# Optimization experiments

Hardware: AMD Instinct MI355X
Metric: run time of the kernel (lower is better)

## Reference

```python
import jax, jax.numpy as jnp
import numpy as np

VOCAB = 1024
EMBED_DIM = 64
COMMIT_COST = 0.25


def setup_inputs() -> dict:
    key = jax.random.key(0)
    k1, k2 = jax.random.split(key)
    z_e = jax.random.normal(k1, (64, 64, 32, 32), dtype=jnp.float32)
    # nn.Embedding init: uniform(-1/vocab, 1/vocab)
    embedding = jax.random.uniform(
        k2, (VOCAB, EMBED_DIM), dtype=jnp.float32,
        minval=-1.0 / VOCAB, maxval=1.0 / VOCAB)
    return {"z_e": z_e, "embedding": embedding}


def reference(z_e, embedding):
    b, d, h, w = z_e.shape
    # [B,D,H,W] -> [N,D]
    flat_z = jnp.transpose(z_e, (0, 2, 3, 1)).reshape(-1, d)
    # squared L2 distances to each code: [N, V]
    distances = (
        jnp.sum(flat_z * flat_z, axis=1, keepdims=True)
        + jnp.sum(embedding * embedding, axis=1)
        - 2.0 * flat_z @ embedding.T
    )
    flat_indices = jnp.argmin(distances, axis=1)
    indices = flat_indices.reshape(b, h, w)
    # gather codes and restore [B,D,H,W]
    z_q = embedding[flat_indices].reshape(b, h, w, d)
    z_q = jnp.transpose(z_q, (0, 3, 1, 2))
    quantization_loss = jnp.mean((z_q - jax.lax.stop_gradient(z_e)) ** 2)
    commitment_loss = jnp.mean((z_e - jax.lax.stop_gradient(z_q)) ** 2) * COMMIT_COST
    z_q_st = z_e + jax.lax.stop_gradient(z_q - z_e)
    # perplexity over codebook usage
    counts = jnp.zeros((VOCAB,), dtype=jnp.float32).at[flat_indices].add(1.0)
    avg_probs = counts / flat_indices.shape[0]
    perplexity = jnp.exp(-jnp.sum(avg_probs * jnp.log(avg_probs + 1e-10)))
    return (z_q_st, indices, quantization_loss, commitment_loss, perplexity)
```

## Files before the change

### kernel.cpp

```cpp
#include <hip/hip_runtime.h>
#include <math.h>

#define VOCAB 1024
#define ED 64
#define NROWS 65536
#define NELEM 4194304
#define MARGIN 2.0e-4f
#define CAPF 8192

typedef __attribute__((ext_vector_type(8))) short short8;
typedef __attribute__((ext_vector_type(4))) float f32x4;

__device__ __forceinline__ unsigned f2bf(float f) {
    unsigned u = __float_as_uint(f);
    u += 0x7fff + ((u >> 16) & 1);
    return u >> 16;
}

__device__ __forceinline__ unsigned long long packkey(float d, int c) {
    unsigned f = __float_as_uint(d);
    unsigned sd = (f & 0x80000000u) ? ~f : (f | 0x80000000u);
    return ((unsigned long long)sd << 32) | (unsigned)c;
}


__global__ void vq_prep(const float* __restrict__ emb, float* __restrict__ e2f,
                        uint4* __restrict__ FB, unsigned* __restrict__ zw1,
                        unsigned* __restrict__ zw2) {
    const int tid = blockIdx.x * 256 + threadIdx.x;
    for (int i = tid; i < 1028; i += 2048) zw1[i] = 0u;
    for (int i = tid; i < 2560; i += 2048) zw2[i] = 0u;

    if (tid < VOCAB) {
        const float4* src = (const float4*)(emb + tid * ED);
        double s = 0.0;
        #pragma unroll
        for (int g = 0; g < 16; ++g) {
            float4 f = src[g];
            s = fma((double)f.x, (double)f.x, s);
            s = fma((double)f.y, (double)f.y, s);
            s = fma((double)f.z, (double)f.z, s);
            s = fma((double)f.w, (double)f.w, s);
        }
        e2f[tid] = (float)s;
    }
    #pragma unroll
    for (int e = 0; e < 4; ++e) {
        const int i = e * 2048 + tid;
        const int n = i & 15, q = (i >> 4) & 3, kh = (i >> 6) & 1, T = i >> 7;
        const int code = T * 16 + n;
        const int k0 = kh * 32 + q * 8;
        const float4* sp = (const float4*)(emb + code * 64 + k0);
        float4 f0 = sp[0], f1 = sp[1];
        uint4 pk;
        pk.x = f2bf(f0.x) | (f2bf(f0.y) << 16);
        pk.y = f2bf(f0.z) | (f2bf(f0.w) << 16);
        pk.z = f2bf(f1.x) | (f2bf(f1.y) << 16);
        pk.w = f2bf(f1.z) | (f2bf(f1.w) << 16);
        FB[i] = pk;
    }
}

__global__ __launch_bounds__(256, 2)
void vq_filter(const float* __restrict__ z, const float* __restrict__ emb,
               const float* __restrict__ e2f, const uint4* __restrict__ FB,
               float* __restrict__ out, double* __restrict__ lossp,
               unsigned* __restrict__ hist, unsigned* __restrict__ nflag,
               unsigned* __restrict__ rowlist) {
    __shared__ uint4 Bs4[4096];
    __shared__ float e2s[1024];
    __shared__ float rowb1[128], rowb2[128];
    __shared__ int   rowi1[128], rowfl[128];
    __shared__ double wls[4];

    const int t = threadIdx.x;
    const int w = t >> 6, lane = t & 63;
    const int q = lane >> 4, n_lo = lane & 15;
    const int bk = blockIdx.x;
    const int n0 = bk * 128;
    const int b  = n0 >> 10;
    const int sb = n0 & 1023;

    #pragma unroll
    for (int i = 0; i < 4; ++i) e2s[i * 256 + t] = e2f[i * 256 + t];

    short8 af[2][2];
    #pragma unroll
    for (int rt = 0; rt < 2; ++rt) {
        const int s = sb + w * 32 + rt * 16 + n_lo;
        const float* zp = z + (size_t)b * 65536 + s;
        #pragma unroll
        for (int kh = 0; kh < 2; ++kh) {
            short8 fr;
            #pragma unroll
            for (int j = 0; j < 8; ++j) {
                int d = kh * 32 + q * 8 + j;
                fr[j] = (short)f2bf(-2.0f * zp[d * 1024]);
            }
            af[rt][kh] = fr;
        }
    }

    float b1[8], b2[8]; int i1[8];
    #pragma unroll
    for (int sl = 0; sl < 8; ++sl) { b1[sl] = 3.4e38f; b2[sl] = 3.4e38f; i1[sl] = 0; }

    const short8* FBs = (const short8*)Bs4;
    for (int h = 0; h < 2; ++h) {
        __syncthreads();
        {
            const uint4* src = FB + h * 4096;
            #pragma unroll
            for (int i = 0; i < 16; ++i) Bs4[i * 256 + t] = src[i * 256 + t];
        }
        __syncthreads();
        #pragma unroll 2
        for (int tt = 0; tt < 32; ++tt) {
            const int T = h * 32 + tt;
            short8 bf0 = FBs[tt * 128 + lane];
            short8 bf1 = FBs[tt * 128 + 64 + lane];
            const int cb = T * 16 + n_lo;
            const float e2 = e2s[cb];
            #pragma unroll
            for (int rt = 0; rt < 2; ++rt) {
                f32x4 a; a[0] = e2; a[1] = e2; a[2] = e2; a[3] = e2;
                a = __builtin_amdgcn_mfma_f32_16x16x32_bf16(af[rt][0], bf0, a, 0, 0, 0);
                a = __builtin_amdgcn_mfma_f32_16x16x32_bf16(af[rt][1], bf1, a, 0, 0, 0);
                #pragma unroll
                for (int reg = 0; reg < 4; ++reg) {
                    const int sl = rt * 4 + reg;
                    float s0 = a[reg];
                    b2[sl] = __builtin_amdgcn_fmed3f(s0, b1[sl], b2[sl]);
                    bool lt = s0 < b1[sl];
                    i1[sl] = lt ? cb : i1[sl];
                    b1[sl] = lt ? s0 : b1[sl];
                }
            }
        }
    }

    #pragma unroll
    for (int m = 1; m < 16; m <<= 1) {
        #pragma unroll
        for (int sl = 0; sl < 8; ++sl) {
            float ob1 = __shfl_xor(b1[sl], m, 64);
            int   oi1 = __shfl_xor(i1[sl], m, 64);
            float ob2 = __shfl_xor(b2[sl], m, 64);
            float lose = fmaxf(b1[sl], ob1);
            b2[sl] = fminf(fminf(b2[sl], ob2), lose);
            bool take = (ob1 < b1[sl]) || (ob1 == b1[sl] && oi1 < i1[sl]);
            b1[sl] = take ? ob1 : b1[sl];
            i1[sl] = take ? oi1 : i1[sl];
        }
    }
    if (n_lo == 0) {
        #pragma unroll
        for (int rt = 0; rt < 2; ++rt) {
            #pragma unroll
            for (int reg = 0; reg < 4; ++reg) {
                int row = w * 32 + rt * 16 + q * 4 + reg;
                int sl = rt * 4 + reg;
                rowb1[row] = b1[sl];
                rowb2[row] = b2[sl];
                rowi1[row] = i1[sl];
            }
        }
    }
    __syncthreads();

    if (t < 128) {
        const int nrow = n0 + t;
        const int code = rowi1[t];
        const bool want = rowb2[t] < rowb1[t] + MARGIN;
        unsigned long long mask = __ballot(want);
        const int cnt = __popcll(mask);
        unsigned base = 0;
        if (lane == 0 && cnt > 0) base = atomicAdd(nflag, (unsigned)cnt);
        base = (unsigned)__shfl((int)base, 0, 64);
        int f = 0;
        if (want) {
            const int rank = __popcll(mask & ((1ULL << lane) - 1ULL));
            const unsigned slot = base + (unsigned)rank;
            if (slot < CAPF) { rowlist[slot] = (unsigned)nrow; f = 1; }
        }
        rowfl[t] = f;
        out[NELEM + nrow] = (float)code;
        if (!f) atomicAdd(&hist[code], 1u);
    }
    __syncthreads();

    {
        const int r = t & 127, tg = t >> 7;
        const int code2 = rowi1[r];
        const bool fl2 = rowfl[r] != 0;
        const int scol = sb + r;
        double lsum = 0.0;
        #pragma unroll
        for (int i = 0; i < 8; ++i) {
            const int d4 = tg * 8 + i;
            float4 e4 = *(const float4*)(emb + code2 * 64 + d4 * 4);
            float es[4] = {e4.x, e4.y, e4.z, e4.w};
            #pragma unroll
            for (int j = 0; j < 4; ++j) {
                int d = d4 * 4 + j;
                size_t off = (size_t)b * 65536 + (size_t)d * 1024 + scol;
                float zv = z[off];
                out[off] = zv + (es[j] - zv);
                double df = (double)es[j] - (double)zv;
                lsum = fma(df, df, lsum);
            }
        }
        if (fl2) lsum = 0.0;
        #pragma unroll
        for (int off = 32; off > 0; off >>= 1)
            lsum += __shfl_down(lsum, off, 64);
        if (lane == 0) wls[w] = lsum;
    }
    __syncthreads();
    if (t == 0) lossp[bk] = wls[0] + wls[1] + wls[2] + wls[3];
}

#define EDOT(i) { \
    const f32x4 a4 = *(const f32x4*)(za + (i) * 4); \
    const f32x4 b4 = *(const f32x4*)(zb + (i) * 4); \
    ma = fmaf(a4[0], e##i[0], ma); ma = fmaf(a4[1], e##i[1], ma); \
    ma = fmaf(a4[2], e##i[2], ma); ma = fmaf(a4[3], e##i[3], ma); \
    mb = fmaf(b4[0], e##i[0], mb); mb = fmaf(b4[1], e##i[1], mb); \
    mb = fmaf(b4[2], e##i[2], mb); mb = fmaf(b4[3], e##i[3], mb); }

__global__ __launch_bounds__(512, 1)
void vq_rescue(const float* __restrict__ z, const float* __restrict__ emb,
               const float* __restrict__ e2f, float* __restrict__ out,
               double* __restrict__ lossp2, unsigned* __restrict__ hist,
               const unsigned* __restrict__ nflag,
               const unsigned* __restrict__ rowlist) {
    __shared__ float zs[32 * 64];
    __shared__ float zns[32];
    __shared__ unsigned long long wkey[16][32];
    __shared__ int rbi[32];
    __shared__ double lred[8];

    const int t = threadIdx.x, w = t >> 6, lane = t & 63;
    const int g = blockIdx.x;
    unsigned nfr = *nflag;
    const int nf = (int)(nfr < CAPF ? nfr : CAPF);
    if (g * 32 >= nf) return;
    const int nloc = (nf - g * 32 < 32) ? (nf - g * 32) : 32;

    {
        const int r = t >> 4, k0 = (t & 15) * 4;
        if (r < nloc) {
            const int row = (int)rowlist[g * 32 + r];
            const int bb = row >> 10, s = row & 1023;
            const float* zp = z + (size_t)bb * 65536 + s;
            #pragma unroll
            for (int k = 0; k < 4; ++k)
                zs[r * 64 + k0 + k] = zp[(size_t)(k0 + k) * 1024];
        }
    }
    __syncthreads();

    if (t < nloc) {
        double a = 0.0;
        for (int k = 0; k < 64; ++k) {
            double v = (double)zs[t * 64 + k];
            a = fma(v, v, a);
        }
        zns[t] = (float)a;
    }
    __syncthreads();

    for (int pass = 0; pass < 2; ++pass) {
        const int c = pass * 512 + w * 64 + lane;
        const f32x4* ep = (const f32x4*)(emb + (size_t)c * 64);
        f32x4 e0 = ep[0],  e1 = ep[1],  e2 = ep[2],  e3 = ep[3];
        f32x4 e4 = ep[4],  e5 = ep[5],  e6 = ep[6],  e7 = ep[7];
        f32x4 e8 = ep[8],  e9 = ep[9],  e10 = ep[10], e11 = ep[11];
        f32x4 e12 = ep[12], e13 = ep[13], e14 = ep[14], e15 = ep[15];
        const float e2c = e2f[c];

        for (int r0 = 0; r0 < nloc; r0 += 2) {
            const bool two = (r0 + 1 < nloc);
            const float* za = zs + r0 * 64;
            const float* zb = zs + (two ? r0 + 1 : r0) * 64;
            float ma = 0.f, mb = 0.f;
            EDOT(0)  EDOT(1)  EDOT(2)  EDOT(3)
            EDOT(4)  EDOT(5)  EDOT(6)  EDOT(7)
            EDOT(8)  EDOT(9)  EDOT(10) EDOT(11)
            EDOT(12) EDOT(13) EDOT(14) EDOT(15)

            const float da = (zns[r0] + e2c) - 2.0f * ma;
            unsigned long long ka = packkey(da, c);
            #pragma unroll
            for (int mo = 32; mo > 0; mo >>= 1) {
                unsigned long long o = __shfl_xor(ka, mo, 64);
                if (o < ka) ka = o;
            }
            unsigned long long kb2 = 0;
            if (two) {
                const float db = (zns[r0 + 1] + e2c) - 2.0f * mb;
                kb2 = packkey(db, c);
                #pragma unroll
                for (int mo = 32; mo > 0; mo >>= 1) {
                    unsigned long long o = __shfl_xor(kb2, mo, 64);
                    if (o < kb2) kb2 = o;
                }
            }
            if (lane == 0) {
                wkey[pass * 8 + w][r0] = ka;
                if (two) wkey[pass * 8 + w][r0 + 1] = kb2;
            }
        }
    }
    __syncthreads();

    if (t < nloc) {
        unsigned long long k0 = wkey[0][t];
        #pragma unroll
        for (int i = 1; i < 16; ++i) {
            unsigned long long ki = wkey[i][t];
            if (ki < k0) k0 = ki;
        }
        const int code = (int)(unsigned)(k0 & 0xffffffffu);
        rbi[t] = code;
        const int row = (int)rowlist[g * 32 + t];
        out[NELEM + row] = (float)code;
        atomicAdd(&hist[code], 1u);
    }
    __syncthreads();

    double lsum = 0.0;
    if (t < 256) {
        const int r = t >> 3, d0 = (t & 7) * 8;
        if (r < nloc) {
            const int row = (int)rowlist[g * 32 + r];
            const int bb = row >> 10, s = row & 1023;
            const int code = rbi[r];
            float4 ea = *(const float4*)(emb + code * 64 + d0);
            float4 eb = *(const float4*)(emb + code * 64 + d0 + 4);
            float es[8] = {ea.x, ea.y, ea.z, ea.w, eb.x, eb.y, eb.z, eb.w};
            #pragma unroll
            for (int j = 0; j < 8; ++j) {
                const int d = d0 + j;
                const size_t off = (size_t)bb * 65536 + (size_t)d * 1024 + s;
                const float zv = zs[r * 64 + d];
                out[off] = zv + (es[j] - zv);
                double df = (double)es[j] - (double)zv;
                lsum = fma(df, df, lsum);
            }
        }
    }
    #pragma unroll
    for (int o = 32; o > 0; o >>= 1) lsum += __shfl_down(lsum, o, 64);
    if (lane == 0) lred[w] = lsum;
    __syncthreads();
    if (t == 0) {
        double s = 0.0;
        #pragma unroll
        for (int i = 0; i < 8; ++i) s += lred[i];
        lossp2[g] = s;
    }
}

__global__ void vq_finalize_kernel(const unsigned* __restrict__ hist,
                                   const double* __restrict__ lossp,
                                   const double* __restrict__ lossp2,
                                   float* __restrict__ out) {
    __shared__ double red[256], red2[256];
    int t = threadIdx.x;
    double ssum = 0.0, lsum = 0.0;
    for (int i = t; i < VOCAB; i += 256) {
        double p = (double)hist[i] / (double)NROWS;
        ssum += p * log(p + 1e-10);
    }
    for (int i = t; i < 1024; i += 256) lsum += lossp[i];
    lsum += lossp2[t];
    red[t] = ssum; red2[t] = lsum;
    __syncthreads();
    for (int off = 128; off > 0; off >>= 1) {
        if (t < off) { red[t] += red[t + off]; red2[t] += red2[t + off]; }
        __syncthreads();
    }
    if (t == 0) {
        double qv = red2[0] / (double)NELEM;
        out[NELEM + NROWS + 0] = (float)qv;
        out[NELEM + NROWS + 1] = (float)(qv * 0.25);
        out[NELEM + NROWS + 2] = (float)exp(-red[0]);
    }
}

extern "C" void kernel_launch(void* const* d_in, const int* in_sizes, int n_in,
                              void* d_out, int out_size, void* d_ws, size_t ws_size,
                              hipStream_t stream) {
    const float* z   = (const float*)d_in[0];
    const float* emb = (const float*)d_in[1];
    float* out = (float*)d_out;

    float*    e2f     = (float*)d_ws;
    unsigned* nfl     = (unsigned*)((char*)d_ws + 4096);
    unsigned* hist    = (unsigned*)((char*)d_ws + 4112);
    unsigned* rowlist = (unsigned*)((char*)d_ws + 8208);
    uint4*    FB      = (uint4*)((char*)d_ws + 40976);
    double*   lossp   = (double*)((char*)d_ws + 172048);
    double*   lossp2  = (double*)((char*)d_ws + 180240);
    unsigned* zw1     = (unsigned*)((char*)d_ws + 4096);
    unsigned* zw2     = (unsigned*)((char*)d_ws + 172048);

    vq_prep<<<dim3(8), dim3(256), 0, stream>>>(emb, e2f, FB, zw1, zw2);
    vq_filter<<<dim3(512), dim3(256), 0, stream>>>(z, emb, e2f, FB, out, lossp,
                                                   hist, nfl, rowlist);
    vq_rescue<<<dim3(256), dim3(512), 0, stream>>>(z, emb, e2f, out, lossp2,
                                                   hist, nfl, rowlist);
    vq_finalize_kernel<<<dim3(1), dim3(256), 0, stream>>>(hist, lossp, lossp2, out);
}
```

Measured before the change: 172.5 us.

## Stage flagged rows contiguously in filter and halve rescue rows per block

The filter kernel now writes each flagged row's z vector into a contiguous workspace buffer at its rowlist slot, so the rescue kernel reads rows contiguously instead of gathering strided columns from z into shared memory. Rescue blocks now handle 16 rows instead of 32, with twice as many blocks, which spreads the exact-rescore work across more CUs. The per-wave argmin now uses a float min-reduce plus a ballot in place of 64-bit key shuffles. The cost is extra global writes in the filter for flagged rows, and z is read from global/L2 inside the dot loop rather than from LDS.

```diff
diff --git a/kernel.cpp b/kernel.cpp
--- a/kernel.cpp
+++ b/kernel.cpp
@@ -29,7 +29,7 @@
                         unsigned* __restrict__ zw2) {
     const int tid = blockIdx.x * 256 + threadIdx.x;
     for (int i = tid; i < 1028; i += 2048) zw1[i] = 0u;
-    for (int i = tid; i < 2560; i += 2048) zw2[i] = 0u;
+    for (int i = tid; i < 3072; i += 2048) zw2[i] = 0u;
 
     if (tid < VOCAB) {
         const float4* src = (const float4*)(emb + tid * ED);
@@ -66,7 +66,7 @@
                const float* __restrict__ e2f, const uint4* __restrict__ FB,
                float* __restrict__ out, double* __restrict__ lossp,
                unsigned* __restrict__ hist, unsigned* __restrict__ nflag,
-               unsigned* __restrict__ rowlist) {
+               unsigned* __restrict__ rowlist, float* __restrict__ zrow) {
     __shared__ uint4 Bs4[4096];
     __shared__ float e2s[1024];
     __shared__ float rowb1[128], rowb2[128];
@@ -177,22 +177,23 @@
         unsigned base = 0;
         if (lane == 0 && cnt > 0) base = atomicAdd(nflag, (unsigned)cnt);
         base = (unsigned)__shfl((int)base, 0, 64);
-        int f = 0;
+        int myslot = -1;
         if (want) {
             const int rank = __popcll(mask & ((1ULL << lane) - 1ULL));
             const unsigned slot = base + (unsigned)rank;
-            if (slot < CAPF) { rowlist[slot] = (unsigned)nrow; f = 1; }
-        }
-        rowfl[t] = f;
+            if (slot < CAPF) { rowlist[slot] = (unsigned)nrow; myslot = (int)slot; }
+        }
+        rowfl[t] = myslot;
         out[NELEM + nrow] = (float)code;
-        if (!f) atomicAdd(&hist[code], 1u);
+        if (myslot < 0) atomicAdd(&hist[code], 1u);
     }
     __syncthreads();
 
     {
         const int r = t & 127, tg = t >> 7;
         const int code2 = rowi1[r];
-        const bool fl2 = rowfl[r] != 0;
+        const int sl2 = rowfl[r];
+        const bool fl2 = sl2 >= 0;
         const int scol = sb + r;
         double lsum = 0.0;
         #pragma unroll
@@ -206,6 +207,7 @@
                 size_t off = (size_t)b * 65536 + (size_t)d * 1024 + scol;
                 float zv = z[off];
                 out[off] = zv + (es[j] - zv);
+                if (fl2) zrow[(size_t)sl2 * 64 + d] = zv;
                 double df = (double)es[j] - (double)zv;
                 lsum = fma(df, df, lsum);
             }
@@ -221,57 +223,42 @@
 }
 
 #define EDOT(i) { \
-    const f32x4 a4 = *(const f32x4*)(za + (i) * 4); \
-    const f32x4 b4 = *(const f32x4*)(zb + (i) * 4); \
-    ma = fmaf(a4[0], e##i[0], ma); ma = fmaf(a4[1], e##i[1], ma); \
-    ma = fmaf(a4[2], e##i[2], ma); ma = fmaf(a4[3], e##i[3], ma); \
-    mb = fmaf(b4[0], e##i[0], mb); mb = fmaf(b4[1], e##i[1], mb); \
-    mb = fmaf(b4[2], e##i[2], mb); mb = fmaf(b4[3], e##i[3], mb); }
+    const float4 a4 = za4[i]; \
+    const float4 b4 = zb4[i]; \
+    ma = fmaf(a4.x, e##i[0], ma); ma = fmaf(a4.y, e##i[1], ma); \
+    ma = fmaf(a4.z, e##i[2], ma); ma = fmaf(a4.w, e##i[3], ma); \
+    mb = fmaf(b4.x, e##i[0], mb); mb = fmaf(b4.y, e##i[1], mb); \
+    mb = fmaf(b4.z, e##i[2], mb); mb = fmaf(b4.w, e##i[3], mb); }
 
 __global__ __launch_bounds__(512, 1)
-void vq_rescue(const float* __restrict__ z, const float* __restrict__ emb,
+void vq_rescue(const float* __restrict__ zrow, const float* __restrict__ emb,
                const float* __restrict__ e2f, float* __restrict__ out,
                double* __restrict__ lossp2, unsigned* __restrict__ hist,
                const unsigned* __restrict__ nflag,
                const unsigned* __restrict__ rowlist) {
-    __shared__ float zs[32 * 64];
-    __shared__ float zns[32];
-    __shared__ unsigned long long wkey[16][32];
-    __shared__ int rbi[32];
+    __shared__ float zns[16];
+    __shared__ unsigned long long wkey[16][16];
+    __shared__ int rbi[16];
     __shared__ double lred[8];
 
     const int t = threadIdx.x, w = t >> 6, lane = t & 63;
     const int g = blockIdx.x;
     unsigned nfr = *nflag;
     const int nf = (int)(nfr < CAPF ? nfr : CAPF);
-    if (g * 32 >= nf) return;
-    const int nloc = (nf - g * 32 < 32) ? (nf - g * 32) : 32;
-
-    {
-        const int r = t >> 4, k0 = (t & 15) * 4;
-        if (r < nloc) {
-            const int row = (int)rowlist[g * 32 + r];
-            const int bb = row >> 10, s = row & 1023;
-            const float* zp = z + (size_t)bb * 65536 + s;
-            #pragma unroll
-            for (int k = 0; k < 4; ++k)
-                zs[r * 64 + k0 + k] = zp[(size_t)(k0 + k) * 1024];
-        }
-    }
-    __syncthreads();
+    if (g * 16 >= nf) return;
+    const int nloc = (nf - g * 16 < 16) ? (nf - g * 16) : 16;
 
     if (t < nloc) {
+        const float* zp = zrow + (size_t)(g * 16 + t) * 64;
         double a = 0.0;
-        for (int k = 0; k < 64; ++k) {
-            double v = (double)zs[t * 64 + k];
-            a = fma(v, v, a);
-        }
+        for (int k = 0; k < 64; ++k) { const double v = (double)zp[k]; a = fma(v, v, a); }
         zns[t] = (float)a;
     }
     __syncthreads();
 
     for (int pass = 0; pass < 2; ++pass) {
-        const int c = pass * 512 + w * 64 + lane;
+        const int cbase = pass * 512 + w * 64;
+        const int c = cbase + lane;
         const f32x4* ep = (const f32x4*)(emb + (size_t)c * 64);
         f32x4 e0 = ep[0],  e1 = ep[1],  e2 = ep[2],  e3 = ep[3];
         f32x4 e4 = ep[4],  e5 = ep[5],  e6 = ep[6],  e7 = ep[7];
@@ -281,34 +268,33 @@
 
         for (int r0 = 0; r0 < nloc; r0 += 2) {
             const bool two = (r0 + 1 < nloc);
-            const float* za = zs + r0 * 64;
-            const float* zb = zs + (two ? r0 + 1 : r0) * 64;
+            const float4* za4 = (const float4*)(zrow + (size_t)(g * 16 + r0) * 64);
+            const float4* zb4 = (const float4*)(zrow + (size_t)(g * 16 + (two ? r0 + 1 : r0)) * 64);
             float ma = 0.f, mb = 0.f;
             EDOT(0)  EDOT(1)  EDOT(2)  EDOT(3)
             EDOT(4)  EDOT(5)  EDOT(6)  EDOT(7)
             EDOT(8)  EDOT(9)  EDOT(10) EDOT(11)
             EDOT(12) EDOT(13) EDOT(14) EDOT(15)
 
-            const float da = (zns[r0] + e2c) - 2.0f * ma;
-            unsigned long long ka = packkey(da, c);
-            #pragma unroll
-            for (int mo = 32; mo > 0; mo >>= 1) {
-                unsigned long long o = __shfl_xor(ka, mo, 64);
-                if (o < ka) ka = o;
-            }
-            unsigned long long kb2 = 0;
+            {
+                const float da = (zns[r0] + e2c) - 2.0f * ma;
+                float dmin = da;
+                #pragma unroll
+                for (int mo = 32; mo > 0; mo >>= 1)
+                    dmin = fminf(dmin, __shfl_xor(dmin, mo, 64));
+                const unsigned long long ball = __ballot(da == dmin);
+                const int wl = __ffsll(ball) - 1;
+                if (lane == 0) wkey[pass * 8 + w][r0] = packkey(dmin, cbase + wl);
+            }
             if (two) {
                 const float db = (zns[r0 + 1] + e2c) - 2.0f * mb;
-                kb2 = packkey(db, c);
+                float dmin = db;
                 #pragma unroll
-                for (int mo = 32; mo > 0; mo >>= 1) {
-                    unsigned long long o = __shfl_xor(kb2, mo, 64);
-                    if (o < kb2) kb2 = o;
-                }
-            }
-            if (lane == 0) {
-                wkey[pass * 8 + w][r0] = ka;
-                if (two) wkey[pass * 8 + w][r0 + 1] = kb2;
+                for (int mo = 32; mo > 0; mo >>= 1)
+                    dmin = fminf(dmin, __shfl_xor(dmin, mo, 64));
+                const unsigned long long ball = __ballot(db == dmin);
+                const int wl = __ffsll(ball) - 1;
+                if (lane == 0) wkey[pass * 8 + w][r0 + 1] = packkey(dmin, cbase + wl);
             }
         }
     }
@@ -323,27 +309,28 @@
         }
         const int code = (int)(unsigned)(k0 & 0xffffffffu);
         rbi[t] = code;
-        const int row = (int)rowlist[g * 32 + t];
+        const int row = (int)rowlist[g * 16 + t];
         out[NELEM + row] = (float)code;
         atomicAdd(&hist[code], 1u);
     }
     __syncthreads();
 
     double lsum = 0.0;
-    if (t < 256) {
+    if (t < 128) {
         const int r = t >> 3, d0 = (t & 7) * 8;
         if (r < nloc) {
-            const int row = (int)rowlist[g * 32 + r];
+            const int row = (int)rowlist[g * 16 + r];
             const int bb = row >> 10, s = row & 1023;
             const int code = rbi[r];
             float4 ea = *(const float4*)(emb + code * 64 + d0);
             float4 eb = *(const float4*)(emb + code * 64 + d0 + 4);
             float es[8] = {ea.x, ea.y, ea.z, ea.w, eb.x, eb.y, eb.z, eb.w};
+            const float* zp = zrow + (size_t)(g * 16 + r) * 64 + d0;
             #pragma unroll
             for (int j = 0; j < 8; ++j) {
                 const int d = d0 + j;
                 const size_t off = (size_t)bb * 65536 + (size_t)d * 1024 + s;
-                const float zv = zs[r * 64 + d];
+                const float zv = zp[j];
                 out[off] = zv + (es[j] - zv);
                 double df = (double)es[j] - (double)zv;
                 lsum = fma(df, df, lsum);
@@ -374,7 +361,7 @@
         ssum += p * log(p + 1e-10);
     }
     for (int i = t; i < 1024; i += 256) lsum += lossp[i];
-    lsum += lossp2[t];
+    for (int i = t; i < 512; i += 256) lsum += lossp2[i];
     red[t] = ssum; red2[t] = lsum;
     __syncthreads();
     for (int off = 128; off > 0; off >>= 1) {
@@ -403,13 +390,14 @@
     uint4*    FB      = (uint4*)((char*)d_ws + 40976);
     double*   lossp   = (double*)((char*)d_ws + 172048);
     double*   lossp2  = (double*)((char*)d_ws + 180240);
+    float*    zrow    = (float*)((char*)d_ws + 184336);
     unsigned* zw1     = (unsigned*)((char*)d_ws + 4096);
     unsigned* zw2     = (unsigned*)((char*)d_ws + 172048);
 
     vq_prep<<<dim3(8), dim3(256), 0, stream>>>(emb, e2f, FB, zw1, zw2);
     vq_filter<<<dim3(512), dim3(256), 0, stream>>>(z, emb, e2f, FB, out, lossp,
-                                                   hist, nfl, rowlist);
-    vq_rescue<<<dim3(256), dim3(512), 0, stream>>>(z, emb, e2f, out, lossp2,
+                                                   hist, nfl, rowlist, zrow);
+    vq_rescue<<<dim3(512), dim3(512), 0, stream>>>(zrow, emb, e2f, out, lossp2,
                                                    hist, nfl, rowlist);
     vq_finalize_kernel<<<dim3(1), dim3(256), 0, stream>>>(hist, lossp, lossp2, out);
 }
```

Result: faster. 158.3 us (-8.2%).
